# Optimization experiments

Hardware: AMD Instinct MI355X
Metric: run time of the kernel (lower is better)

Reference implementation:

```python
import jax, jax.numpy as jnp
import numpy as np

D_MODEL = 256
D_HIDDEN = 1024
B, S = 4, 32768


def setup_inputs() -> dict:
    key = jax.random.key(0)
    k_x, k_m, k_w1, k_b1, k_w2, k_b2 = jax.random.split(key, 6)
    x = jax.random.normal(k_x, (B, S, D_MODEL), dtype=jnp.float32)
    # graph_dependency: binary connectivity mask [d_hidden, d_model]
    mask = jax.random.randint(k_m, (D_HIDDEN, D_MODEL), 0, 2, dtype=jnp.int32)
    lim1 = 1.0 / np.sqrt(D_MODEL)
    lim2 = 1.0 / np.sqrt(D_HIDDEN)
    w1 = jax.random.uniform(k_w1, (D_HIDDEN, D_MODEL), jnp.float32, -lim1, lim1)
    b1 = jax.random.uniform(k_b1, (D_HIDDEN,), jnp.float32, -lim1, lim1)
    # reserve=True: maps d_hidden -> d_model with transposed mask
    w2 = jax.random.uniform(k_w2, (D_MODEL, D_HIDDEN), jnp.float32, -lim2, lim2)
    b2 = jax.random.uniform(k_b2, (D_MODEL,), jnp.float32, -lim2, lim2)
    return {"x": x, "w1": w1, "b1": b1, "w2": w2, "b2": b2, "mask": mask}


def reference(x, w1, b1, w2, b2, mask):
    m = mask.astype(x.dtype)                      # [H, D]
    # fc1: graph-masked linear d_model -> d_hidden
    h = jnp.einsum('bsd,hd->bsh', x, w1 * m) + b1  # [B, S, H]
    h = jax.nn.relu(h)
    # fc2 (reserve): graph-masked linear d_hidden -> d_model, transposed mask
    y = jnp.einsum('bsh,dh->bsd', h, w2 * m.T) + b2  # [B, S, D]
    return y
```

## Files before the change

kernel.cpp:

```cpp
#include <hip/hip_runtime.h>


#define D_MODEL 256
#define D_HID   1024
#define MT      128
#define NCHUNK  32
#define CHUNK_ELEMS 8192

typedef __attribute__((ext_vector_type(8))) short short8;
typedef __attribute__((ext_vector_type(16))) float f32x16;
typedef __attribute__((ext_vector_type(4))) unsigned int uint4v;

__device__ __forceinline__ unsigned short f2bf(float f) {
  union { float f; unsigned int u; } v; v.f = f;
  unsigned int u = v.u;
  return (unsigned short)((u + 0x7FFFu + ((u >> 16) & 1u)) >> 16);
}

__device__ __forceinline__ unsigned cvtpk_bf16(float lo, float hi) {
  unsigned r;
  asm("v_cvt_pk_bf16_f32 %0, %1, %2" : "=v"(r) : "v"(lo), "v"(hi));
  return r;
}

__device__ __forceinline__ void plswap(unsigned &a, unsigned &b) {
  asm("v_permlane32_swap_b32 %0, %1" : "+v"(a), "+v"(b));
}

__device__ __forceinline__ void async16(void* lds, const void* g) {
  __builtin_amdgcn_global_load_lds(
      (const __attribute__((address_space(1))) unsigned int*)g,
      (__attribute__((address_space(3))) unsigned int*)lds,
      16, 0, 0);
}

__global__ __launch_bounds__(256) void prep_weights(
    const float* __restrict__ w1, const float* __restrict__ w2,
    const int* __restrict__ mask,
    unsigned short* __restrict__ W1p, unsigned short* __restrict__ W2p)
{
  int t = blockIdx.x * 256 + threadIdx.x;
  if (t < 32768) {
    int c    = t >> 10;
    int kf   = (t >> 6) & 15;
    int lane = t & 63;
    int h = c * 32 + (lane & 31);
    int k = kf * 16 + (lane >> 5) * 8;
    const float* wp = w1 + h * 256 + k;
    const int*   mp = mask + h * 256 + k;
    short8 v;
    #pragma unroll
    for (int j = 0; j < 8; ++j) v[j] = (short)(mp[j] ? f2bf(wp[j]) : 0);
    *(short8*)(W1p + (size_t)t * 8) = v;
  } else {
    int s    = t - 32768;
    int c    = s >> 10;
    int cf   = (s >> 7) & 7;
    int kf2  = (s >> 6) & 1;
    int lane = s & 63;
    int n = cf * 32 + (lane & 31);
    int h = c * 32 + kf2 * 16 + (lane >> 5) * 8;
    short8 v;
    #pragma unroll
    for (int j = 0; j < 8; ++j)
      v[j] = (short)(mask[(h + j) * 256 + n] ? f2bf(w2[n * 1024 + h + j]) : 0);
    *(short8*)(W2p + (size_t)s * 8) = v;
  }
}

__global__ __launch_bounds__(256, 2) void ffd_fused(
    const float* __restrict__ X, const float* __restrict__ b1,
    const float* __restrict__ b2,
    const unsigned short* __restrict__ W1p, const unsigned short* __restrict__ W2p,
    float* __restrict__ Y)
{
  __shared__ unsigned short sW1[2][CHUNK_ELEMS];
  __shared__ unsigned short sW2[2][CHUNK_ELEMS];
  __shared__ float sB1[D_HID];

  const int tid  = threadIdx.x;
  const int lane = tid & 63;
  const int w    = tid >> 6;
  const int l32  = lane & 31;
  const int q2   = lane >> 5;

  const long rowBase = (long)blockIdx.x * MT + w * 32;

  short8 xf[16];
  const float* xrow = X + (rowBase + l32) * D_MODEL;
  #pragma unroll
  for (int kf = 0; kf < 16; ++kf) {
    const float4 f0 = *(const float4*)(xrow + kf * 16 + q2 * 8);
    const float4 f1 = *(const float4*)(xrow + kf * 16 + q2 * 8 + 4);
    short8 v;
    v[0] = (short)f2bf(f0.x); v[1] = (short)f2bf(f0.y);
    v[2] = (short)f2bf(f0.z); v[3] = (short)f2bf(f0.w);
    v[4] = (short)f2bf(f1.x); v[5] = (short)f2bf(f1.y);
    v[6] = (short)f2bf(f1.z); v[7] = (short)f2bf(f1.w);
    xf[kf] = v;
  }

  f32x16 acc[8];
  #pragma unroll
  for (int i = 0; i < 8; ++i)
    #pragma unroll
    for (int j = 0; j < 16; ++j) acc[i][j] = 0.f;

  async16(&sB1[tid * 4], b1 + tid * 4);
  {
    const unsigned short* g1 = W1p + tid * 8;
    const unsigned short* g2 = W2p + tid * 8;
    #pragma unroll
    for (int i = 0; i < 4; ++i) {
      async16(&sW1[0][i * 2048 + tid * 8], g1 + i * 2048);
      async16(&sW2[0][i * 2048 + tid * 8], g2 + i * 2048);
    }
  }
  __syncthreads();

  for (int c = 0; c < NCHUNK; ++c) {
    const int cur = c & 1;

    if (c + 1 < NCHUNK) {
      const unsigned short* g1 = W1p + (size_t)(c + 1) * CHUNK_ELEMS + tid * 8;
      const unsigned short* g2 = W2p + (size_t)(c + 1) * CHUNK_ELEMS + tid * 8;
      unsigned short* d1 = &sW1[cur ^ 1][tid * 8];
      unsigned short* d2 = &sW2[cur ^ 1][tid * 8];
      #pragma unroll
      for (int i = 0; i < 4; ++i) {
        async16(d1 + i * 2048, g1 + i * 2048);
        async16(d2 + i * 2048, g2 + i * 2048);
      }
    }

    float4 bb[4];
    #pragma unroll
    for (int g = 0; g < 4; ++g)
      bb[g] = *(const float4*)&sB1[c * 32 + 4 * q2 + 8 * g];

    f32x16 h0, h1;
    #pragma unroll
    for (int j = 0; j < 16; ++j) { h0[j] = 0.f; h1[j] = 0.f; }
    __builtin_amdgcn_s_setprio(1);
    #pragma unroll
    for (int kf = 0; kf < 8; ++kf) {
      short8 wa = *(const short8*)&sW1[cur][kf * 512 + lane * 8];
      short8 wb = *(const short8*)&sW1[cur][(kf + 8) * 512 + lane * 8];
      h0 = __builtin_amdgcn_mfma_f32_32x32x16_bf16(wa, xf[kf],     h0, 0, 0, 0);
      h1 = __builtin_amdgcn_mfma_f32_32x32x16_bf16(wb, xf[kf + 8], h1, 0, 0, 0);
    }
    __builtin_amdgcn_s_setprio(0);

    float v[16];
    #pragma unroll
    for (int r = 0; r < 16; ++r) {
      float t = h0[r] + h1[r] + bb[r >> 2][r & 3];
      v[r] = t > 0.f ? t : 0.f;
    }

    unsigned W0 = cvtpk_bf16(v[0],  v[1]),  W1 = cvtpk_bf16(v[2],  v[3]);
    unsigned W2 = cvtpk_bf16(v[4],  v[5]),  W3 = cvtpk_bf16(v[6],  v[7]);
    unsigned W4 = cvtpk_bf16(v[8],  v[9]),  W5 = cvtpk_bf16(v[10], v[11]);
    unsigned W6 = cvtpk_bf16(v[12], v[13]), W7 = cvtpk_bf16(v[14], v[15]);
    plswap(W0, W2); plswap(W1, W3); plswap(W4, W6); plswap(W5, W7);
    union { uint4v u; short8 s; } A0, A1;
    A0.u = (uint4v){W0, W1, W2, W3};
    A1.u = (uint4v){W4, W5, W6, W7};

    __builtin_amdgcn_s_setprio(1);
    #pragma unroll
    for (int cf = 0; cf < 8; ++cf) {
      short8 b0 = *(const short8*)&sW2[cur][(cf * 2 + 0) * 512 + lane * 8];
      short8 b1f = *(const short8*)&sW2[cur][(cf * 2 + 1) * 512 + lane * 8];
      acc[cf] = __builtin_amdgcn_mfma_f32_32x32x16_bf16(A0.s, b0,  acc[cf], 0, 0, 0);
      acc[cf] = __builtin_amdgcn_mfma_f32_32x32x16_bf16(A1.s, b1f, acc[cf], 0, 0, 0);
    }
    __builtin_amdgcn_s_setprio(0);

    __syncthreads();
  }

  #pragma unroll
  for (int cf = 0; cf < 8; ++cf) {
    int col = cf * 32 + l32;
    float bias = b2[col];
    #pragma unroll
    for (int r = 0; r < 16; ++r) {
      long row = rowBase + (r & 3) + 8 * (r >> 2) + 4 * q2;
      Y[row * D_MODEL + col] = acc[cf][r] + bias;
    }
  }
}

extern "C" void kernel_launch(void* const* d_in, const int* in_sizes, int n_in,
                              void* d_out, int out_size, void* d_ws, size_t ws_size,
                              hipStream_t stream) {
  const float* x    = (const float*)d_in[0];
  const float* w1   = (const float*)d_in[1];
  const float* b1   = (const float*)d_in[2];
  const float* w2   = (const float*)d_in[3];
  const float* b2   = (const float*)d_in[4];
  const int*   mask = (const int*)d_in[5];

  unsigned short* W1p = (unsigned short*)d_ws;
  unsigned short* W2p = W1p + (size_t)D_HID * D_MODEL;
  float* Y = (float*)d_out;

  prep_weights<<<256, 256, 0, stream>>>(w1, w2, mask, W1p, W2p);
  ffd_fused<<<131072 / MT, 256, 0, stream>>>(x, b1, b2, W1p, W2p, Y);
}
```

Before: 163.8 us.

## Replace double-buffered weight prefetch with single-buffer two-chunk phases

The loop now runs 16 phases instead of 32 chunks. Each phase loads two consecutive weight chunks into one LDS buffer, synchronizes, and computes both chunks. This halves the barrier count and load/sync overhead per chunk, but removes the overlap of the next chunk's loads with current compute. Occupancy is meant to come from two blocks per CU, which overlap each other's load stalls instead.

```diff
diff --git a/kernel.cpp b/kernel.cpp
--- a/kernel.cpp
+++ b/kernel.cpp
@@ -4,8 +4,8 @@
 #define D_MODEL 256
 #define D_HID   1024
 #define MT      128
-#define NCHUNK  32
-#define CHUNK_ELEMS 8192
+#define NPHASE  16
+#define SUBC_ELEMS 8192
 
 typedef __attribute__((ext_vector_type(8))) short short8;
 typedef __attribute__((ext_vector_type(16))) float f32x16;
@@ -74,8 +74,8 @@
     const unsigned short* __restrict__ W1p, const unsigned short* __restrict__ W2p,
     float* __restrict__ Y)
 {
-  __shared__ unsigned short sW1[2][CHUNK_ELEMS];
-  __shared__ unsigned short sW2[2][CHUNK_ELEMS];
+  __shared__ unsigned short sW1[2 * SUBC_ELEMS];
+  __shared__ unsigned short sW2[2 * SUBC_ELEMS];
   __shared__ float sB1[D_HID];
 
   const int tid  = threadIdx.x;
@@ -107,77 +107,72 @@
     for (int j = 0; j < 16; ++j) acc[i][j] = 0.f;
 
   async16(&sB1[tid * 4], b1 + tid * 4);
-  {
-    const unsigned short* g1 = W1p + tid * 8;
-    const unsigned short* g2 = W2p + tid * 8;
-    #pragma unroll
-    for (int i = 0; i < 4; ++i) {
-      async16(&sW1[0][i * 2048 + tid * 8], g1 + i * 2048);
-      async16(&sW2[0][i * 2048 + tid * 8], g2 + i * 2048);
-    }
-  }
-  __syncthreads();
-
-  for (int c = 0; c < NCHUNK; ++c) {
-    const int cur = c & 1;
-
-    if (c + 1 < NCHUNK) {
-      const unsigned short* g1 = W1p + (size_t)(c + 1) * CHUNK_ELEMS + tid * 8;
-      const unsigned short* g2 = W2p + (size_t)(c + 1) * CHUNK_ELEMS + tid * 8;
-      unsigned short* d1 = &sW1[cur ^ 1][tid * 8];
-      unsigned short* d2 = &sW2[cur ^ 1][tid * 8];
-      #pragma unroll
-      for (int i = 0; i < 4; ++i) {
+
+  for (int C = 0; C < NPHASE; ++C) {
+    __syncthreads();
+    {
+      const unsigned short* g1 = W1p + (size_t)C * (2 * SUBC_ELEMS) + tid * 8;
+      const unsigned short* g2 = W2p + (size_t)C * (2 * SUBC_ELEMS) + tid * 8;
+      unsigned short* d1 = &sW1[tid * 8];
+      unsigned short* d2 = &sW2[tid * 8];
+      #pragma unroll
+      for (int i = 0; i < 8; ++i) {
         async16(d1 + i * 2048, g1 + i * 2048);
         async16(d2 + i * 2048, g2 + i * 2048);
       }
     }
-
-    float4 bb[4];
-    #pragma unroll
-    for (int g = 0; g < 4; ++g)
-      bb[g] = *(const float4*)&sB1[c * 32 + 4 * q2 + 8 * g];
-
-    f32x16 h0, h1;
-    #pragma unroll
-    for (int j = 0; j < 16; ++j) { h0[j] = 0.f; h1[j] = 0.f; }
-    __builtin_amdgcn_s_setprio(1);
-    #pragma unroll
-    for (int kf = 0; kf < 8; ++kf) {
-      short8 wa = *(const short8*)&sW1[cur][kf * 512 + lane * 8];
-      short8 wb = *(const short8*)&sW1[cur][(kf + 8) * 512 + lane * 8];
-      h0 = __builtin_amdgcn_mfma_f32_32x32x16_bf16(wa, xf[kf],     h0, 0, 0, 0);
-      h1 = __builtin_amdgcn_mfma_f32_32x32x16_bf16(wb, xf[kf + 8], h1, 0, 0, 0);
+    __syncthreads();
+
+    #pragma unroll
+    for (int p = 0; p < 2; ++p) {
+      const int c = C * 2 + p;
+      const unsigned short* w1c = &sW1[p * SUBC_ELEMS];
+      const unsigned short* w2c = &sW2[p * SUBC_ELEMS];
+
+      float4 bb[4];
+      #pragma unroll
+      for (int g = 0; g < 4; ++g)
+        bb[g] = *(const float4*)&sB1[c * 32 + 4 * q2 + 8 * g];
+
+      f32x16 h0, h1;
+      #pragma unroll
+      for (int j = 0; j < 16; ++j) { h0[j] = 0.f; h1[j] = 0.f; }
+      __builtin_amdgcn_s_setprio(1);
+      #pragma unroll
+      for (int kf = 0; kf < 8; ++kf) {
+        short8 wa = *(const short8*)&w1c[kf * 512 + lane * 8];
+        short8 wb = *(const short8*)&w1c[(kf + 8) * 512 + lane * 8];
+        h0 = __builtin_amdgcn_mfma_f32_32x32x16_bf16(wa, xf[kf],     h0, 0, 0, 0);
+        h1 = __builtin_amdgcn_mfma_f32_32x32x16_bf16(wb, xf[kf + 8], h1, 0, 0, 0);
+      }
+      __builtin_amdgcn_s_setprio(0);
+
+      float v[16];
+      #pragma unroll
+      for (int r = 0; r < 16; ++r) {
+        float t = h0[r] + h1[r] + bb[r >> 2][r & 3];
+        v[r] = t > 0.f ? t : 0.f;
+      }
+
+      unsigned W0 = cvtpk_bf16(v[0],  v[1]),  W1 = cvtpk_bf16(v[2],  v[3]);
+      unsigned W2 = cvtpk_bf16(v[4],  v[5]),  W3 = cvtpk_bf16(v[6],  v[7]);
+      unsigned W4 = cvtpk_bf16(v[8],  v[9]),  W5 = cvtpk_bf16(v[10], v[11]);
+      unsigned W6 = cvtpk_bf16(v[12], v[13]), W7 = cvtpk_bf16(v[14], v[15]);
+      plswap(W0, W2); plswap(W1, W3); plswap(W4, W6); plswap(W5, W7);
+      union { uint4v u; short8 s; } A0, A1;
+      A0.u = (uint4v){W0, W1, W2, W3};
+      A1.u = (uint4v){W4, W5, W6, W7};
+
+      __builtin_amdgcn_s_setprio(1);
+      #pragma unroll
+      for (int cf = 0; cf < 8; ++cf) {
+        short8 b0  = *(const short8*)&w2c[(cf * 2 + 0) * 512 + lane * 8];
+        short8 b1f = *(const short8*)&w2c[(cf * 2 + 1) * 512 + lane * 8];
+        acc[cf] = __builtin_amdgcn_mfma_f32_32x32x16_bf16(A0.s, b0,  acc[cf], 0, 0, 0);
+        acc[cf] = __builtin_amdgcn_mfma_f32_32x32x16_bf16(A1.s, b1f, acc[cf], 0, 0, 0);
+      }
+      __builtin_amdgcn_s_setprio(0);
     }
-    __builtin_amdgcn_s_setprio(0);
-
-    float v[16];
-    #pragma unroll
-    for (int r = 0; r < 16; ++r) {
-      float t = h0[r] + h1[r] + bb[r >> 2][r & 3];
-      v[r] = t > 0.f ? t : 0.f;
-    }
-
-    unsigned W0 = cvtpk_bf16(v[0],  v[1]),  W1 = cvtpk_bf16(v[2],  v[3]);
-    unsigned W2 = cvtpk_bf16(v[4],  v[5]),  W3 = cvtpk_bf16(v[6],  v[7]);
-    unsigned W4 = cvtpk_bf16(v[8],  v[9]),  W5 = cvtpk_bf16(v[10], v[11]);
-    unsigned W6 = cvtpk_bf16(v[12], v[13]), W7 = cvtpk_bf16(v[14], v[15]);
-    plswap(W0, W2); plswap(W1, W3); plswap(W4, W6); plswap(W5, W7);
-    union { uint4v u; short8 s; } A0, A1;
-    A0.u = (uint4v){W0, W1, W2, W3};
-    A1.u = (uint4v){W4, W5, W6, W7};
-
-    __builtin_amdgcn_s_setprio(1);
-    #pragma unroll
-    for (int cf = 0; cf < 8; ++cf) {
-      short8 b0 = *(const short8*)&sW2[cur][(cf * 2 + 0) * 512 + lane * 8];
-      short8 b1f = *(const short8*)&sW2[cur][(cf * 2 + 1) * 512 + lane * 8];
-      acc[cf] = __builtin_amdgcn_mfma_f32_32x32x16_bf16(A0.s, b0,  acc[cf], 0, 0, 0);
-      acc[cf] = __builtin_amdgcn_mfma_f32_32x32x16_bf16(A1.s, b1f, acc[cf], 0, 0, 0);
-    }
-    __builtin_amdgcn_s_setprio(0);
-
-    __syncthreads();
   }
 
   #pragma unroll
```

Measured after the change: 160.0 us. 1.02x faster.
